# Kernel optimization log

Hardware: AMD Instinct MI355X
Metric: run time of the kernel (lower is better)

The kernel has to match this reference:

```python
import jax, jax.numpy as jnp
import numpy as np
from jax import lax


def _sweep(u, w, V, axis, reverse):
    """One directional min-sum DP sweep (SGM recurrence).

    u: (B, CV, H, W, D) unary costs
    w: (B, 1, H, W)     per-pixel edge weights for this direction
    V: (D, D)           label-context (pairwise smoothness) matrix
    axis: spatial axis of u to scan along (2 = H, 3 = W)
    reverse: scan in decreasing index order
    Returns L: (B, CV, H, W, D) aggregated directional costs,
    L(p, l) = u(p, l) + min_{l'} [ L(p-d, l') + w(p) * V(l', l) ],
    with L = u at the border.
    """
    if reverse:
        u = jnp.flip(u, axis)
        w = jnp.flip(w, axis)
    u_s = jnp.moveaxis(u, axis, 0)   # (T, B, CV, P, D)
    w_s = jnp.moveaxis(w, axis, 0)   # (T, B, 1, P)

    init = u_s[0]

    def step(L_prev, xs):
        u_t, w_t = xs
        # cand[..., l', l] = L_prev[..., l'] + w_t * V[l', l]
        cand = L_prev[..., :, None] + w_t[..., None, None] * V
        L = u_t + jnp.min(cand, axis=-2)
        return L, L

    _, Ls = lax.scan(step, init, (u_s[1:], w_s[1:]))
    L_all = jnp.concatenate([init[None], Ls], axis=0)
    L_all = jnp.moveaxis(L_all, 0, axis)
    if reverse:
        L_all = jnp.flip(L_all, axis)
    return L_all


def setup_inputs() -> dict:
    key = jax.random.key(0)
    k1, k2, k3 = jax.random.split(key, 3)
    B, CV, D, H, W = 4, 1, 21, 512, 512
    N_DIR = 4
    unary = jax.random.uniform(k1, (B, CV, D, H, W), dtype=jnp.float32)
    edge_weights = jax.random.uniform(k2, (B, N_DIR, H, W), dtype=jnp.float32)
    label_context = jax.random.uniform(k3, (D, D), dtype=jnp.float32)
    return {"unary": unary, "edge_weights": edge_weights,
            "label_context": label_context}


def reference(unary, edge_weights, label_context):
    # unary: (B, CV, D, H, W) -> (B, CV, H, W, D) as in MPModule.forward
    u = jnp.transpose(unary, (0, 1, 3, 4, 2))
    # directions: 0 = left->right, 1 = right->left, 2 = top->down, 3 = bottom->up
    dir_cfg = [(3, False), (3, True), (2, False), (2, True)]
    n_dir = len(dir_cfg)
    cost = u
    for d, (axis, reverse) in enumerate(dir_cfg):
        w_d = edge_weights[:, d][:, None]  # (B, 1, H, W)
        L_d = _sweep(u, w_d, label_context, axis, reverse)
        cost = cost + (L_d - u)  # accumulate directional messages
    # permute back to (B, CV, D, H, W) as the module does
    return jnp.transpose(cost, (0, 1, 4, 2, 3))
```

## Files before the change

### kernel.cpp

```cpp
#include <hip/hip_runtime.h>


#define DLBL 21
#define SP 512
#define NB 4
#define SPSP ((long)SP * SP)
#define NELEM ((long)NB * DLBL * SP * SP)

__global__ __launch_bounds__(256)
void transpose2_kernel(const float* __restrict__ u, const float* __restrict__ ew,
                       float* __restrict__ uT, float* l2t, float* l3t)
{
    __shared__ float tile[32][33];
    const int plane = blockIdx.z;
    const float* src;
    float* dst;
    if (plane < NB * DLBL) {
        src = u  + (long)plane * SPSP;
        dst = uT + (long)plane * SPSP;
    } else {
        const int q = plane - NB * DLBL;
        const int b = q >> 1, db = q & 1;
        src = ew + (long)(b * 4 + 2 + db) * SPSP;
        dst = (db ? l3t : l2t) + (long)(b * DLBL + 20) * SPSP;
    }
    const int x0 = blockIdx.x * 32, y0 = blockIdx.y * 32;
    const int tx = threadIdx.x & 31, ty = threadIdx.x >> 5;
#pragma unroll
    for (int j = 0; j < 4; ++j)
        tile[ty + 8 * j][tx] = src[(long)(y0 + ty + 8 * j) * SP + (x0 + tx)];
    __syncthreads();
#pragma unroll
    for (int j = 0; j < 4; ++j)
        dst[(long)(x0 + ty + 8 * j) * SP + (y0 + tx)] = tile[tx][ty + 8 * j];
}

__global__ __launch_bounds__(64, 3)
void sweep4(const float* __restrict__ unary, const float* __restrict__ ew,
            const float* __restrict__ Vmat, const float* __restrict__ uT,
            float* __restrict__ out, float* __restrict__ l1,
            float* l2t, float* l3t)
{
    __shared__ float xch[4][24];
    __shared__ float stage[4][693];
    const int lane = threadIdx.x;
    const int g    = lane / DLBL;
    const int s    = lane - g * DLBL;
    int taskId = blockIdx.x * 3 + (g < 3 ? g : 0);
    if (taskId >= 8192) taskId = 8191;

    const int dir  = taskId >> 11;
    const int line = taskId & 2047;
    const int b    = line >> 9;
    const int p    = line & (SP - 1);
    const int axis = dir >> 1;
    const int rev  = dir & 1;
    const float usub = (dir == 0) ? 0.0f : 1.0f;

    float Vc[DLBL];
#pragma unroll
    for (int j = 0; j < DLBL; ++j) Vc[j] = Vmat[j * DLBL + s];

    const float4* ub4 = (const float4*)((axis ? uT : unary)
                        + (long)(b * DLBL + s) * SPSP + (long)p * SP);
    const float* wbase = axis
        ? ((dir == 2 ? l2t : l3t) + (long)(b * DLBL + 20) * SPSP + (long)p * SP)
        : (ew + (long)(b * 4 + dir) * SPSP + (long)p * SP);
    const float4* wb4 = (const float4*)wbase;

    const int frow = lane >> 5, fcol = lane & 31;
    const int stbase = s * 33;

    float* fb[3]; int wrev[3]; bool fvalid[3];
#pragma unroll
    for (int gg = 0; gg < 3; ++gg) {
        const int tid = blockIdx.x * 3 + gg;
        fvalid[gg] = (tid < 8192);
        const int tid2 = fvalid[gg] ? tid : 8191;
        const int d_ = tid2 >> 11;
        const int ln = tid2 & 2047;
        const int bb = ln >> 9;
        const int pp = ln & (SP - 1);
        wrev[gg] = d_ & 1;
        float* dst = (d_ == 0) ? out : (d_ == 1) ? l1 : (d_ == 2) ? l2t : l3t;
        fb[gg] = dst + (long)(bb * DLBL) * SPSP + (long)pp * SP + (long)frow * SPSP;
    }

    float4 uS0[4], uS1[4], uS2[4], uS3[4];
    float4 wS0[4], wS1[4], wS2[4], wS3[4];
    float cur = 0.0f;

#define QIDX(bi, k) (rev ? (127 - 4 * (bi) - (k)) : (4 * (bi) + (k)))

#define LOADU(bi, U) do {                                                   \
    _Pragma("unroll")                                                       \
    for (int k = 0; k < 4; ++k) U[k] = ub4[QIDX(bi, k)];                    \
    } while (0)

#define LOADW(bi, W) do {                                                   \
    _Pragma("unroll")                                                       \
    for (int k = 0; k < 4; ++k) W[k] = wb4[QIDX(bi, k)];                    \
    } while (0)

#define PROC(bi, U, W, FIRSTB) do {                                         \
    _Pragma("unroll")                                                       \
    for (int k = 0; k < 4; ++k) {                                           \
        const float ua_[4] = {U[k].x, U[k].y, U[k].z, U[k].w};              \
        const float wa_[4] = {W[k].x, W[k].y, W[k].z, W[k].w};              \
        const int q_ = QIDX(bi, k);                                         \
        _Pragma("unroll")                                                   \
        for (int j = 0; j < 4; ++j) {                                       \
            const int   jc  = rev ? 3 - j : j;                              \
            const float u_c = ua_[jc];                                      \
            const float w_c = wa_[jc];                                      \
            const int   t   = q_ * 4 + jc;                                  \
            xch[g][s] = cur;                                                \
            __builtin_amdgcn_wave_barrier();                                \
            float Lp[24];                                                   \
            _Pragma("unroll")                                               \
            for (int qq = 0; qq < 6; ++qq)                                  \
                ((float4*)Lp)[qq] = ((const float4*)(&xch[g][0]))[qq];      \
            __builtin_amdgcn_wave_barrier();                                \
            float c[DLBL];                                                  \
            _Pragma("unroll")                                               \
            for (int jj = 0; jj < DLBL; ++jj)                               \
                c[jj] = fmaf(w_c, Vc[jj], Lp[jj]);                          \
            float m7[7];                                                    \
            _Pragma("unroll")                                               \
            for (int kk = 0; kk < 7; ++kk)                                  \
                m7[kk] = fminf(fminf(c[3*kk], c[3*kk+1]), c[3*kk+2]);       \
            const float ma = fminf(fminf(m7[0], m7[1]), m7[2]);             \
            const float mb = fminf(fminf(m7[3], m7[4]), m7[5]);             \
            const float nv = u_c + fminf(fminf(ma, mb), m7[6]);             \
            cur = ((FIRSTB) && k == 0 && j == 0) ? u_c : nv;                \
            stage[g][stbase + (t & 31)] = fmaf(-usub, u_c, cur);            \
        }                                                                   \
    } } while (0)

#define FLW(w_) do {                                                        \
    __builtin_amdgcn_wave_barrier();                                        \
    _Pragma("unroll")                                                       \
    for (int gg = 0; gg < 3; ++gg) {                                        \
        if (fvalid[gg]) {                                                   \
            float* bp = fb[gg] + (wrev[gg] ? (480 - 32 * (w_))              \
                                           : (32 * (w_)));                  \
            _Pragma("unroll")                                               \
            for (int r2 = 0; r2 < 11; ++r2) {                               \
                const int rr = 2 * r2 + frow;                               \
                if (rr < DLBL) bp[fcol] = stage[gg][rr * 33 + fcol];        \
                bp += 2 * SPSP;                                             \
            }                                                               \
        }                                                                   \
    }                                                                       \
    __builtin_amdgcn_wave_barrier();                                        \
} while (0)

    LOADU(0, uS0); LOADW(0, wS0);
    LOADU(1, uS1); LOADW(1, wS1);
    LOADU(2, uS2); LOADW(2, wS2);
    LOADU(3, uS3); LOADW(3, wS3);

    for (int ww = 0; ww < 8; ++ww) {
        const int B0 = 4 * ww;
        PROC(B0 + 0, uS0, wS0, (ww == 0));
        if (B0 + 4 < 32) { LOADU(B0 + 4, uS0); LOADW(B0 + 4, wS0); }
        PROC(B0 + 1, uS1, wS1, false);
        if (B0 + 5 < 32) { LOADU(B0 + 5, uS1); LOADW(B0 + 5, wS1); }
        FLW(2 * ww);
        PROC(B0 + 2, uS2, wS2, false);
        if (B0 + 6 < 32) { LOADU(B0 + 6, uS2); LOADW(B0 + 6, wS2); }
        PROC(B0 + 3, uS3, wS3, false);
        if (B0 + 7 < 32) { LOADU(B0 + 7, uS3); LOADW(B0 + 7, wS3); }
        FLW(2 * ww + 1);
    }

#undef QIDX
#undef LOADU
#undef LOADW
#undef PROC
#undef FLW
}

__global__ __launch_bounds__(256)
void finish_kernel(const float* __restrict__ l1, const float* __restrict__ l2t,
                   const float* __restrict__ l3t, float* __restrict__ out)
{
    __shared__ float t2[32][33], t3[32][33];
    const long pb = (long)blockIdx.z * SPSP;
    const int x0 = blockIdx.x * 32, y0 = blockIdx.y * 32;
    const int tx = threadIdx.x & 31, ty = threadIdx.x >> 5;
#pragma unroll
    for (int j = 0; j < 4; ++j) {
        const long o = pb + (long)(x0 + ty + 8 * j) * SP + (y0 + tx);
        t2[ty + 8 * j][tx] = l2t[o];
        t3[ty + 8 * j][tx] = l3t[o];
    }
    __syncthreads();
#pragma unroll
    for (int j = 0; j < 4; ++j) {
        const long o = pb + (long)(y0 + ty + 8 * j) * SP + (x0 + tx);
        out[o] = out[o] + l1[o] + t2[tx][ty + 8 * j] + t3[tx][ty + 8 * j];
    }
}

template<int MODE>
__global__ __launch_bounds__(64)
void sweep_fb(const float* __restrict__ unary, const float* __restrict__ ew,
              const float* __restrict__ Vmat, float* __restrict__ out,
              int taskBase)
{
    __shared__ float xch[4][24];
    const int lane = threadIdx.x;
    const int g    = lane / DLBL;
    const int s    = lane - g * DLBL;
    int local = blockIdx.x * 3 + (g < 3 ? g : 0);
    const bool valid = (g < 3) && (local < 2048);
    if (local >= 2048) local = 2047;
    const int taskId = taskBase + local;
    const int dir  = taskId >> 11;
    const int line = taskId & 2047;
    const int b = line >> 9, p = line & (SP - 1);
    const int axis = dir >> 1, rev = dir & 1;

    float Vc[DLBL];
#pragma unroll
    for (int j = 0; j < DLBL; ++j) Vc[j] = Vmat[j * DLBL + s];

    const long ustep = axis ? SP : 1;
    const long ubase = (long)(b * DLBL + s) * SPSP + (axis ? (long)p : (long)p * SP);
    const long wbase = (long)(b * 4 + dir) * SPSP + (axis ? (long)p : (long)p * SP);
    const long uoff  = rev ? -ustep : ustep;
    const long ust   = rev ? (long)(SP - 1) * ustep : 0;

    const float* up = unary + ubase + ust;
    const float* wp = ew    + wbase + ust;
    float*       op = out   + ubase + ust;

    float cur = up[0];
    if (valid && MODE == 1) *op = cur;

    float ub0 = up[uoff], ub1 = up[2*uoff], ub2 = up[3*uoff], ub3 = up[4*uoff];
    float wb0 = wp[uoff], wb1 = wp[2*uoff], wb2 = wp[3*uoff], wb3 = wp[4*uoff];
    float ob0 = 0, ob1 = 0, ob2 = 0, ob3 = 0;
    if (MODE == 2) { ob0 = op[uoff]; ob1 = op[2*uoff]; ob2 = op[3*uoff]; ob3 = op[4*uoff]; }
    const float* upf = up + 4 * uoff;
    const float* wpf = wp + 4 * uoff;
    const float* opf = op + 4 * uoff;

    for (int t = 1; t < SP; ++t) {
        const float u_c = ub0, w_c = wb0, o_c = ob0;
        ub0 = ub1; ub1 = ub2; ub2 = ub3;
        wb0 = wb1; wb1 = wb2; wb2 = wb3;
        if (MODE == 2) { ob0 = ob1; ob1 = ob2; ob2 = ob3; }
        const bool adv = (t + 4) < SP;
        upf += adv ? uoff : 0; wpf += adv ? uoff : 0;
        ub3 = *upf; wb3 = *wpf;
        if (MODE == 2) { opf += adv ? uoff : 0; ob3 = *opf; }

        xch[g][s] = cur;
        __builtin_amdgcn_wave_barrier();
        float Lp[24];
#pragma unroll
        for (int q = 0; q < 6; ++q)
            ((float4*)Lp)[q] = ((const float4*)(&xch[g][0]))[q];
        __builtin_amdgcn_wave_barrier();

        float c[DLBL];
#pragma unroll
        for (int j = 0; j < DLBL; ++j) c[j] = fmaf(w_c, Vc[j], Lp[j]);
        float m7[7];
#pragma unroll
        for (int k = 0; k < 7; ++k)
            m7[k] = fminf(fminf(c[3*k], c[3*k+1]), c[3*k+2]);
        const float ma = fminf(fminf(m7[0], m7[1]), m7[2]);
        const float mb = fminf(fminf(m7[3], m7[4]), m7[5]);
        cur = u_c + fminf(fminf(ma, mb), m7[6]);

        op += uoff;
        if (valid) *op = (MODE == 2) ? (o_c + cur - u_c) : cur;
    }
}

extern "C" void kernel_launch(void* const* d_in, const int* in_sizes, int n_in,
                              void* d_out, int out_size, void* d_ws, size_t ws_size,
                              hipStream_t stream) {
    const float* unary = (const float*)d_in[0];
    const float* ew    = (const float*)d_in[1];
    const float* Vmat  = (const float*)d_in[2];
    float* o = (float*)d_out;

    const size_t needA = (size_t)(4 * NELEM) * sizeof(float);

    if (ws_size >= needA) {
        float* uT  = (float*)d_ws;
        float* l1  = uT + NELEM;
        float* l2t = l1 + NELEM;
        float* l3t = l2t + NELEM;

        dim3 tg(16, 16, NB * DLBL + 8);
        transpose2_kernel<<<tg, 256, 0, stream>>>(unary, ew, uT, l2t, l3t);

        const int grid = (8192 + 2) / 3;
        sweep4<<<grid, 64, 0, stream>>>(unary, ew, Vmat, uT,
                                        o, l1, l2t, l3t);

        finish_kernel<<<dim3(16, 16, NB * DLBL), 256, 0, stream>>>(l1, l2t, l3t, o);
    } else {
        const int grid = (2048 + 2) / 3;
        sweep_fb<1><<<grid, 64, 0, stream>>>(unary, ew, Vmat, o, 0);
        for (int d = 1; d < 4; ++d)
            sweep_fb<2><<<grid, 64, 0, stream>>>(unary, ew, Vmat, o, d * 2048);
    }
}
```

Before: 554.9 us.

## Vectorize transpose/finish kernels, interleave sweep tasks, branchless prefetch, lower occupancy hint

The transpose and finish kernels now use float4 global loads and stores with a padded 36-wide shared tile in place of scalar 32x33 tiles. Sweep tasks are remapped so forward and reverse directions interleave across blocks, and the prefetch macro clamps its index so the conditional loads go away. The launch bound drops from 3 to 2 waves per SIMD, which gives the sweep kernel more registers but may reduce occupancy. The padded float4 tile layout may bring back some shared-memory bank conflicts.

```diff
diff --git a/kernel.cpp b/kernel.cpp
--- a/kernel.cpp
+++ b/kernel.cpp
@@ -7,11 +7,17 @@
 #define SPSP ((long)SP * SP)
 #define NELEM ((long)NB * DLBL * SP * SP)
 
+__device__ __forceinline__ void map_task(int i, int& dir, int& line)
+{
+    if (i < 4096) { dir = i & 1;       line = i >> 1; }
+    else          { const int j = i - 4096; dir = 2 + (j & 1); line = j >> 1; }
+}
+
 __global__ __launch_bounds__(256)
 void transpose2_kernel(const float* __restrict__ u, const float* __restrict__ ew,
                        float* __restrict__ uT, float* l2t, float* l3t)
 {
-    __shared__ float tile[32][33];
+    __shared__ float tile[32][36];
     const int plane = blockIdx.z;
     const float* src;
     float* dst;
@@ -25,18 +31,21 @@
         dst = (db ? l3t : l2t) + (long)(b * DLBL + 20) * SPSP;
     }
     const int x0 = blockIdx.x * 32, y0 = blockIdx.y * 32;
-    const int tx = threadIdx.x & 31, ty = threadIdx.x >> 5;
-#pragma unroll
-    for (int j = 0; j < 4; ++j)
-        tile[ty + 8 * j][tx] = src[(long)(y0 + ty + 8 * j) * SP + (x0 + tx)];
+    const int r  = threadIdx.x >> 3;
+    const int c4 = (threadIdx.x & 7) * 4;
+    const float4 v = *(const float4*)&src[(long)(y0 + r) * SP + (x0 + c4)];
+    *(float4*)&tile[r][c4] = v;
     __syncthreads();
-#pragma unroll
-    for (int j = 0; j < 4; ++j)
-        dst[(long)(x0 + ty + 8 * j) * SP + (y0 + tx)] = tile[tx][ty + 8 * j];
-}
-
-__global__ __launch_bounds__(64, 3)
-void sweep4(const float* __restrict__ unary, const float* __restrict__ ew,
+    float4 ov;
+    ov.x = tile[c4 + 0][r];
+    ov.y = tile[c4 + 1][r];
+    ov.z = tile[c4 + 2][r];
+    ov.w = tile[c4 + 3][r];
+    *(float4*)&dst[(long)(x0 + r) * SP + (y0 + c4)] = ov;
+}
+
+__global__ __launch_bounds__(64, 2)
+void sweep5(const float* __restrict__ unary, const float* __restrict__ ew,
             const float* __restrict__ Vmat, const float* __restrict__ uT,
             float* __restrict__ out, float* __restrict__ l1,
             float* l2t, float* l3t)
@@ -49,8 +58,8 @@
     int taskId = blockIdx.x * 3 + (g < 3 ? g : 0);
     if (taskId >= 8192) taskId = 8191;
 
-    const int dir  = taskId >> 11;
-    const int line = taskId & 2047;
+    int dir, line;
+    map_task(taskId, dir, line);
     const int b    = line >> 9;
     const int p    = line & (SP - 1);
     const int axis = dir >> 1;
@@ -76,9 +85,8 @@
     for (int gg = 0; gg < 3; ++gg) {
         const int tid = blockIdx.x * 3 + gg;
         fvalid[gg] = (tid < 8192);
-        const int tid2 = fvalid[gg] ? tid : 8191;
-        const int d_ = tid2 >> 11;
-        const int ln = tid2 & 2047;
+        int d_, ln;
+        map_task(fvalid[gg] ? tid : 8191, d_, ln);
         const int bb = ln >> 9;
         const int pp = ln & (SP - 1);
         wrev[gg] = d_ & 1;
@@ -92,15 +100,13 @@
 
 #define QIDX(bi, k) (rev ? (127 - 4 * (bi) - (k)) : (4 * (bi) + (k)))
 
-#define LOADU(bi, U) do {                                                   \
+#define LOADB(bi_, U, W) do {                                               \
+    const int bq_ = ((bi_) > 31) ? 31 : (bi_);                              \
     _Pragma("unroll")                                                       \
-    for (int k = 0; k < 4; ++k) U[k] = ub4[QIDX(bi, k)];                    \
-    } while (0)
-
-#define LOADW(bi, W) do {                                                   \
-    _Pragma("unroll")                                                       \
-    for (int k = 0; k < 4; ++k) W[k] = wb4[QIDX(bi, k)];                    \
-    } while (0)
+    for (int k = 0; k < 4; ++k) {                                           \
+        const int q_ = QIDX(bq_, k);                                        \
+        U[k] = ub4[q_]; W[k] = wb4[q_];                                     \
+    } } while (0)
 
 #define PROC(bi, U, W, FIRSTB) do {                                         \
     _Pragma("unroll")                                                       \
@@ -155,28 +161,27 @@
     __builtin_amdgcn_wave_barrier();                                        \
 } while (0)
 
-    LOADU(0, uS0); LOADW(0, wS0);
-    LOADU(1, uS1); LOADW(1, wS1);
-    LOADU(2, uS2); LOADW(2, wS2);
-    LOADU(3, uS3); LOADW(3, wS3);
+    LOADB(0, uS0, wS0);
+    LOADB(1, uS1, wS1);
+    LOADB(2, uS2, wS2);
+    LOADB(3, uS3, wS3);
 
     for (int ww = 0; ww < 8; ++ww) {
         const int B0 = 4 * ww;
         PROC(B0 + 0, uS0, wS0, (ww == 0));
-        if (B0 + 4 < 32) { LOADU(B0 + 4, uS0); LOADW(B0 + 4, wS0); }
+        LOADB(B0 + 4, uS0, wS0);
         PROC(B0 + 1, uS1, wS1, false);
-        if (B0 + 5 < 32) { LOADU(B0 + 5, uS1); LOADW(B0 + 5, wS1); }
+        LOADB(B0 + 5, uS1, wS1);
         FLW(2 * ww);
         PROC(B0 + 2, uS2, wS2, false);
-        if (B0 + 6 < 32) { LOADU(B0 + 6, uS2); LOADW(B0 + 6, wS2); }
+        LOADB(B0 + 6, uS2, wS2);
         PROC(B0 + 3, uS3, wS3, false);
-        if (B0 + 7 < 32) { LOADU(B0 + 7, uS3); LOADW(B0 + 7, wS3); }
+        LOADB(B0 + 7, uS3, wS3);
         FLW(2 * ww + 1);
     }
 
 #undef QIDX
-#undef LOADU
-#undef LOADW
+#undef LOADB
 #undef PROC
 #undef FLW
 }
@@ -185,22 +190,24 @@
 void finish_kernel(const float* __restrict__ l1, const float* __restrict__ l2t,
                    const float* __restrict__ l3t, float* __restrict__ out)
 {
-    __shared__ float t2[32][33], t3[32][33];
+    __shared__ float t2[32][36], t3[32][36];
     const long pb = (long)blockIdx.z * SPSP;
     const int x0 = blockIdx.x * 32, y0 = blockIdx.y * 32;
-    const int tx = threadIdx.x & 31, ty = threadIdx.x >> 5;
-#pragma unroll
-    for (int j = 0; j < 4; ++j) {
-        const long o = pb + (long)(x0 + ty + 8 * j) * SP + (y0 + tx);
-        t2[ty + 8 * j][tx] = l2t[o];
-        t3[ty + 8 * j][tx] = l3t[o];
-    }
+    const int r  = threadIdx.x >> 3;
+    const int c4 = (threadIdx.x & 7) * 4;
+    const float4 v2 = *(const float4*)&l2t[pb + (long)(x0 + r) * SP + (y0 + c4)];
+    const float4 v3 = *(const float4*)&l3t[pb + (long)(x0 + r) * SP + (y0 + c4)];
+    *(float4*)&t2[r][c4] = v2;
+    *(float4*)&t3[r][c4] = v3;
     __syncthreads();
-#pragma unroll
-    for (int j = 0; j < 4; ++j) {
-        const long o = pb + (long)(y0 + ty + 8 * j) * SP + (x0 + tx);
-        out[o] = out[o] + l1[o] + t2[tx][ty + 8 * j] + t3[tx][ty + 8 * j];
-    }
+    const long o = pb + (long)(y0 + r) * SP + (x0 + c4);
+    const float4 a = *(const float4*)&l1[o];
+    float4 ov = *(const float4*)&out[o];
+    ov.x += a.x + t2[c4 + 0][r] + t3[c4 + 0][r];
+    ov.y += a.y + t2[c4 + 1][r] + t3[c4 + 1][r];
+    ov.z += a.z + t2[c4 + 2][r] + t3[c4 + 2][r];
+    ov.w += a.w + t2[c4 + 3][r] + t3[c4 + 3][r];
+    *(float4*)&out[o] = ov;
 }
 
 template<int MODE>
@@ -301,7 +308,7 @@
         transpose2_kernel<<<tg, 256, 0, stream>>>(unary, ew, uT, l2t, l3t);
 
         const int grid = (8192 + 2) / 3;
-        sweep4<<<grid, 64, 0, stream>>>(unary, ew, Vmat, uT,
+        sweep5<<<grid, 64, 0, stream>>>(unary, ew, Vmat, uT,
                                         o, l1, l2t, l3t);
 
         finish_kernel<<<dim3(16, 16, NB * DLBL), 256, 0, stream>>>(l1, l2t, l3t, o);
```

Result: faster. 477.5 us (-14.0%).
